# Performance work log

Hardware: AMD Instinct MI355X
Metric: run time of the kernel (lower is better)

## Reference

```python
import jax, jax.numpy as jnp
import numpy as np


def euler_xyz_to_matrix(angles):
    # pytorch3d euler_angles_to_matrix(angles, 'XYZ') = R_X(a0) @ R_Y(a1) @ R_Z(a2)
    ax, ay, az = angles[..., 0], angles[..., 1], angles[..., 2]
    cx, sx = jnp.cos(ax), jnp.sin(ax)
    cy, sy = jnp.cos(ay), jnp.sin(ay)
    cz, sz = jnp.cos(az), jnp.sin(az)
    one = jnp.ones_like(ax)
    zero = jnp.zeros_like(ax)
    Rx = jnp.stack([one, zero, zero, zero, cx, -sx, zero, sx, cx], axis=-1).reshape(*ax.shape, 3, 3)
    Ry = jnp.stack([cy, zero, sy, zero, one, zero, -sy, zero, cy], axis=-1).reshape(*ax.shape, 3, 3)
    Rz = jnp.stack([cz, -sz, zero, sz, cz, zero, zero, zero, one], axis=-1).reshape(*ax.shape, 3, 3)
    return Rx @ Ry @ Rz


def chamfer_bidir(x, y):
    # x, y: [R, I, N, 3]. Squared-distance chamfer, mean point reduction, per (R,I) batch.
    x2 = jnp.sum(x * x, axis=-1)  # [R,I,N]
    y2 = jnp.sum(y * y, axis=-1)  # [R,I,N]
    # d2[r,i,n,m] = |x_n - y_m|^2
    d2 = x2[..., :, None] + y2[..., None, :] - 2.0 * jnp.einsum('rind,rimd->rinm', x, y)
    cham_x = jnp.mean(jnp.min(d2, axis=-1), axis=-1)  # x -> nearest y
    cham_y = jnp.mean(jnp.min(d2, axis=-2), axis=-1)  # y -> nearest x
    return cham_x + cham_y  # [R, I]


def setup_inputs() -> dict:
    key = jax.random.key(0)
    k1, k2, k3, k4 = jax.random.split(key, 4)
    R, I, N = 4, 16, 2048
    source_points = jax.random.normal(k1, (R, I, N, 3), dtype=jnp.float32)
    target_points = jax.random.normal(k2, (I, N, 3), dtype=jnp.float32)
    rotation = 0.1 * jax.random.normal(k3, (R, I, 3), dtype=jnp.float32)
    translation = 0.1 * jax.random.normal(k4, (R, I, 3), dtype=jnp.float32)
    scale = jnp.ones((R, I), dtype=jnp.float32)
    return {
        'source_points': source_points,
        'target_points': target_points,
        'rotation': rotation,
        'translation': translation,
        'scale': scale,
    }


def reference(source_points, target_points, rotation, translation, scale):
    R, I, N, _ = source_points.shape
    rot = euler_xyz_to_matrix(rotation)  # [R,I,3,3]
    # Transform per original: 4x4 matrix with rows [:3,:] scaled by `scale`,
    # so p' = scale * (rot @ p + translation).
    transformed = scale[..., None, None] * (
        jnp.einsum('rind,rikd->rink', source_points, rot) + translation[..., None, :]
    )  # [R,I,N,3]
    # target_points [I,N,3] broadcast to [R,I,N,3] (original repeats along R)
    target = jnp.broadcast_to(target_points[None], transformed.shape)
    # original calls chamfer_distance(target, transformed): x=target, y=transformed
    return chamfer_bidir(target, transformed)  # [R, I]
```

## Files before the change

kernel.cpp:

```cpp
#include <hip/hip_runtime.h>
#include <math.h>

#define RDIM 4
#define IDIM 16
#define NPAIR 64
#define NPTS 2048
#define THREADS 256
#define ROWSB 256
#define RBLK (NPTS / ROWSB)
#define T16 (NPTS / 16)
#define PSPLIT 4
#define ONEBF 0x3F80u

typedef __attribute__((ext_vector_type(8))) short bf16x8;
typedef __attribute__((ext_vector_type(4))) float f32x4;

__device__ __forceinline__ float min3f(float a, float b, float c) {
    return fminf(a, fminf(b, c));
}

__device__ __forceinline__ unsigned int f2bf(float f) {
    union { float f; unsigned int u; } v; v.f = f;
    return (v.u + 0x7FFFu + ((v.u >> 16) & 1u)) >> 16;
}
__device__ __forceinline__ float bf2f(unsigned int h) {
    union { unsigned int u; float f; } v; v.u = h << 16; return v.f;
}

__device__ __forceinline__ void make_rot(const float* __restrict__ rotv, int pair,
                                         float& r00, float& r01, float& r02,
                                         float& r10, float& r11, float& r12,
                                         float& r20, float& r21, float& r22) {
    const float ax = rotv[pair * 3 + 0];
    const float ay = rotv[pair * 3 + 1];
    const float az = rotv[pair * 3 + 2];
    float sx, cx, sy, cy, sz, cz;
    sincosf(ax, &sx, &cx);
    sincosf(ay, &sy, &cy);
    sincosf(az, &sz, &cz);
    r00 = cy * cz;                r01 = -cy * sz;               r02 = sy;
    r10 = cx * sz + sx * sy * cz; r11 = cx * cz - sx * sy * sz; r12 = -sx * cy;
    r20 = sx * sz - cx * sy * cz; r21 = sx * cz + cx * sy * sz; r22 = cx * cy;
}

__device__ __forceinline__ uint4 brec(float v0, float v1, float v2) {
    const float b0 = -2.0f * v0, b1 = -2.0f * v1, b2 = -2.0f * v2;
    const unsigned int h0 = f2bf(b0), h1 = f2bf(b1), h2 = f2bf(b2);
    const unsigned int l0 = f2bf(b0 - bf2f(h0));
    const unsigned int l1 = f2bf(b1 - bf2f(h1));
    const unsigned int l2 = f2bf(b2 - bf2f(h2));
    const float n2 = v0 * v0 + v1 * v1 + v2 * v2;
    const unsigned int nh = f2bf(n2), nl = f2bf(n2 - bf2f(nh));
    return make_uint4(h0 | (h1 << 16), h2 | (l0 << 16), l1 | (l2 << 16), nh | (nl << 16));
}
__device__ __forceinline__ void arec(float q0, float q1, float q2, uint4& a0, uint4& a1) {
    const unsigned int h0 = f2bf(q0), h1 = f2bf(q1), h2 = f2bf(q2);
    const unsigned int l0 = f2bf(q0 - bf2f(h0));
    const unsigned int l1 = f2bf(q1 - bf2f(h1));
    const unsigned int l2 = f2bf(q2 - bf2f(h2));
    a0 = make_uint4(h0 | (h1 << 16), h2 | (l0 << 16), l1 | (l2 << 16), ONEBF);
    a1 = make_uint4(l0 | (l1 << 16), l2 | (h0 << 16), h1 | (h2 << 16), ONEBF << 16);
}

__global__ __launch_bounds__(THREADS)
void prep(const float* __restrict__ src, const float* __restrict__ tgt,
          const float* __restrict__ rotv, const float* __restrict__ trav,
          const float* __restrict__ scal,
          uint4* __restrict__ Yb, uint4* __restrict__ Ya,
          uint4* __restrict__ Xb, uint4* __restrict__ Xa)
{
    const int b   = blockIdx.x;
    const int seg = blockIdx.y;
    const int tid = threadIdx.x;
    const int m0  = seg * (NPTS / PSPLIT);
    if (b < NPAIR) {
        const int pair = b;
        float r00, r01, r02, r10, r11, r12, r20, r21, r22;
        make_rot(rotv, pair, r00, r01, r02, r10, r11, r12, r20, r21, r22);
        const float t0 = trav[pair * 3 + 0];
        const float t1 = trav[pair * 3 + 1];
        const float t2 = trav[pair * 3 + 2];
        const float s  = scal[pair];
        const float* __restrict__ srcp = src + (size_t)pair * NPTS * 3;
#pragma unroll
        for (int u = 0; u < NPTS / THREADS / PSPLIT; ++u) {
            const int m = m0 + u * THREADS + tid;
            const float p0 = srcp[m * 3 + 0];
            const float p1 = srcp[m * 3 + 1];
            const float p2 = srcp[m * 3 + 2];
            const float y0 = s * fmaf(r00, p0, fmaf(r01, p1, fmaf(r02, p2, t0)));
            const float y1 = s * fmaf(r10, p0, fmaf(r11, p1, fmaf(r12, p2, t1)));
            const float y2 = s * fmaf(r20, p0, fmaf(r21, p1, fmaf(r22, p2, t2)));
            Yb[(size_t)pair * NPTS + m] = brec(y0, y1, y2);
            uint4 a0, a1;
            arec(y0, y1, y2, a0, a1);
            Ya[((size_t)pair * NPTS + m) * 2 + 0] = a0;
            Ya[((size_t)pair * NPTS + m) * 2 + 1] = a1;
        }
    } else {
        const int i = b - NPAIR;
        const float* __restrict__ tgtp = tgt + (size_t)i * NPTS * 3;
#pragma unroll
        for (int u = 0; u < NPTS / THREADS / PSPLIT; ++u) {
            const int m = m0 + u * THREADS + tid;
            const float x0 = tgtp[m * 3 + 0];
            const float x1 = tgtp[m * 3 + 1];
            const float x2 = tgtp[m * 3 + 2];
            Xb[(size_t)i * NPTS + m] = brec(x0, x1, x2);
            uint4 a0, a1;
            arec(x0, x1, x2, a0, a1);
            Xa[((size_t)i * NPTS + m) * 2 + 0] = a0;
            Xa[((size_t)i * NPTS + m) * 2 + 1] = a1;
        }
    }
}

__global__ __launch_bounds__(THREADS, 4)
void chamfer_main(const uint4* __restrict__ Yb, const uint4* __restrict__ Ya,
                  const uint4* __restrict__ Xb, const uint4* __restrict__ Xa,
                  float* __restrict__ out, const float czero)
{
    __shared__ alignas(16) unsigned char smem[32768];
    __shared__ float rowmin[ROWSB];
    __shared__ float wsum[4];
    unsigned short* sB = (unsigned short*)smem;

    const int pair  = blockIdx.x;
    const int rb    = blockIdx.y;
    const int passB = blockIdx.z;
    const int i     = pair & (IDIM - 1);
    const int tid   = threadIdx.x;
    const int lane  = tid & 63;
    const int w     = tid >> 6;
    const int c15   = lane & 15;
    const int hi    = lane >> 4;

    const uint4* __restrict__ gB = (passB == 0) ? (Yb + (size_t)pair * NPTS)
                                                : (Xb + (size_t)i * NPTS);
    const uint4* __restrict__ gA = (passB == 0)
        ? (Xa + ((size_t)i * NPTS + rb * ROWSB) * 2)
        : (Ya + ((size_t)pair * NPTS + rb * ROWSB) * 2);
    const char* gAb = (const char*)gA;

#pragma unroll
    for (int j = 0; j < 8; ++j)
        ((uint4*)sB)[j * THREADS + tid] = gB[j * THREADS + tid];

    const bf16x8 zero8 = {0, 0, 0, 0, 0, 0, 0, 0};
    bf16x8 af[4];
#pragma unroll
    for (int rt = 0; rt < 4; ++rt) {
        const int row = w * 64 + rt * 16 + c15;
        af[rt] = (hi < 2) ? *(const bf16x8*)(gAb + row * 32 + hi * 16) : zero8;
    }

    f32x4 zero4;
    zero4[0] = czero; zero4[1] = czero; zero4[2] = czero; zero4[3] = czero;

    float mn[4][4];
#pragma unroll
    for (int rt = 0; rt < 4; ++rt)
#pragma unroll
        for (int j = 0; j < 4; ++j) mn[rt][j] = 3.4e38f;

    __syncthreads();

#pragma unroll 2
    for (int t = 0; t < T16; t += 2) {
        const bf16x8 bf0 = *(const bf16x8*)&sB[((t + 0) * 16 + c15) * 8];
        const bf16x8 bf1 = *(const bf16x8*)&sB[((t + 1) * 16 + c15) * 8];
#pragma unroll
        for (int rt = 0; rt < 4; ++rt) {
            const f32x4 d0 = __builtin_amdgcn_mfma_f32_16x16x32_bf16(af[rt], bf0, zero4, 0, 0, 0);
            const f32x4 d1 = __builtin_amdgcn_mfma_f32_16x16x32_bf16(af[rt], bf1, zero4, 0, 0, 0);
#pragma unroll
            for (int j = 0; j < 4; ++j)
                mn[rt][j] = min3f(mn[rt][j], d0[j], d1[j]);
        }
    }

#pragma unroll
    for (int rt = 0; rt < 4; ++rt)
#pragma unroll
        for (int j = 0; j < 4; ++j) {
            float v = mn[rt][j];
            v = fminf(v, __shfl_xor(v, 1, 64));
            v = fminf(v, __shfl_xor(v, 2, 64));
            v = fminf(v, __shfl_xor(v, 4, 64));
            v = fminf(v, __shfl_xor(v, 8, 64));
            mn[rt][j] = v;
        }

    if (c15 == 0) {
#pragma unroll
        for (int rt = 0; rt < 4; ++rt) {
            f32x4 v4;
            v4[0] = mn[rt][0]; v4[1] = mn[rt][1];
            v4[2] = mn[rt][2]; v4[3] = mn[rt][3];
            *(f32x4*)&rowmin[w * 64 + rt * 16 + hi * 4] = v4;
        }
    }
    __syncthreads();

    const float m = rowmin[tid];
    const unsigned short* ar = (const unsigned short*)(gAb + tid * 32);
    const float q0 = bf2f(ar[0]) + bf2f(ar[3]);
    const float q1 = bf2f(ar[1]) + bf2f(ar[4]);
    const float q2 = bf2f(ar[2]) + bf2f(ar[5]);
    float v = m + q0 * q0 + q1 * q1 + q2 * q2;

#pragma unroll
    for (int off = 32; off > 0; off >>= 1)
        v += __shfl_down(v, off, 64);
    if (lane == 0) wsum[w] = v;
    __syncthreads();
    if (tid == 0) {
        const float tot = wsum[0] + wsum[1] + wsum[2] + wsum[3];
        atomicAdd(&out[pair], tot * (1.0f / NPTS));
    }
}

extern "C" void kernel_launch(void* const* d_in, const int* in_sizes, int n_in,
                              void* d_out, int out_size, void* d_ws, size_t ws_size,
                              hipStream_t stream) {
    const float* src  = (const float*)d_in[0];
    const float* tgt  = (const float*)d_in[1];
    const float* rotv = (const float*)d_in[2];
    const float* trav = (const float*)d_in[3];
    const float* scal = (const float*)d_in[4];
    float* out = (float*)d_out;

    char* ws = (char*)d_ws;
    uint4* Yb = (uint4*)ws;
    uint4* Ya = (uint4*)(ws + (size_t)NPAIR * NPTS * 16);
    uint4* Xb = (uint4*)(ws + (size_t)NPAIR * NPTS * 48);
    uint4* Xa = (uint4*)(ws + (size_t)NPAIR * NPTS * 48 + (size_t)IDIM * NPTS * 16);

    hipMemsetAsync(out, 0, NPAIR * sizeof(float), stream);

    dim3 pgrid(NPAIR + IDIM, PSPLIT);
    prep<<<pgrid, THREADS, 0, stream>>>(src, tgt, rotv, trav, scal, Yb, Ya, Xb, Xa);

    dim3 grid(NPAIR, RBLK, 2);
    chamfer_main<<<grid, THREADS, 0, stream>>>(Yb, Ya, Xb, Xa, out, 0.0f);
}
```

Baseline: 105.5 us.

## Switch chamfer MFMA to 32x32x16 tiles with software-pipelined min reduction

Result: faster. 85.79 us (median of 2 runs) (-18.7%).

```diff
diff --git a/kernel.cpp b/kernel.cpp
--- a/kernel.cpp
+++ b/kernel.cpp
@@ -8,11 +8,12 @@
 #define THREADS 256
 #define ROWSB 256
 #define RBLK (NPTS / ROWSB)
-#define T16 (NPTS / 16)
+#define TILES (NPTS / 32)
 #define PSPLIT 4
 #define ONEBF 0x3F80u
 
 typedef __attribute__((ext_vector_type(8))) short bf16x8;
+typedef __attribute__((ext_vector_type(16))) float f32x16;
 typedef __attribute__((ext_vector_type(4))) float f32x4;
 
 __device__ __forceinline__ float min3f(float a, float b, float c) {
@@ -67,11 +68,13 @@
           const float* __restrict__ rotv, const float* __restrict__ trav,
           const float* __restrict__ scal,
           uint4* __restrict__ Yb, uint4* __restrict__ Ya,
-          uint4* __restrict__ Xb, uint4* __restrict__ Xa)
+          uint4* __restrict__ Xb, uint4* __restrict__ Xa,
+          float* __restrict__ out)
 {
     const int b   = blockIdx.x;
     const int seg = blockIdx.y;
     const int tid = threadIdx.x;
+    if (b == 0 && seg == 0 && tid < NPAIR) out[tid] = 0.0f;
     const int m0  = seg * (NPTS / PSPLIT);
     if (b < NPAIR) {
         const int pair = b;
@@ -115,7 +118,7 @@
     }
 }
 
-__global__ __launch_bounds__(THREADS, 4)
+__global__ __launch_bounds__(THREADS, 3)
 void chamfer_main(const uint4* __restrict__ Yb, const uint4* __restrict__ Ya,
                   const uint4* __restrict__ Xb, const uint4* __restrict__ Xa,
                   float* __restrict__ out, const float czero)
@@ -132,8 +135,8 @@
     const int tid   = threadIdx.x;
     const int lane  = tid & 63;
     const int w     = tid >> 6;
-    const int c15   = lane & 15;
-    const int hi    = lane >> 4;
+    const int c31   = lane & 31;
+    const int h     = lane >> 5;
 
     const uint4* __restrict__ gB = (passB == 0) ? (Yb + (size_t)pair * NPTS)
                                                 : (Xb + (size_t)i * NPTS);
@@ -146,58 +149,73 @@
     for (int j = 0; j < 8; ++j)
         ((uint4*)sB)[j * THREADS + tid] = gB[j * THREADS + tid];
 
-    const bf16x8 zero8 = {0, 0, 0, 0, 0, 0, 0, 0};
-    bf16x8 af[4];
-#pragma unroll
-    for (int rt = 0; rt < 4; ++rt) {
-        const int row = w * 64 + rt * 16 + c15;
-        af[rt] = (hi < 2) ? *(const bf16x8*)(gAb + row * 32 + hi * 16) : zero8;
-    }
-
-    f32x4 zero4;
-    zero4[0] = czero; zero4[1] = czero; zero4[2] = czero; zero4[3] = czero;
-
-    float mn[4][4];
-#pragma unroll
-    for (int rt = 0; rt < 4; ++rt)
-#pragma unroll
-        for (int j = 0; j < 4; ++j) mn[rt][j] = 3.4e38f;
+    const bf16x8 af0 = *(const bf16x8*)(gAb + (w * 64 + c31) * 32 + h * 16);
+    const bf16x8 af1 = *(const bf16x8*)(gAb + (w * 64 + 32 + c31) * 32 + h * 16);
+
+    f32x16 czv;
+#pragma unroll
+    for (int j = 0; j < 16; ++j) czv[j] = czero;
+
+    float mn0[16], mn1[16];
+#pragma unroll
+    for (int j = 0; j < 16; ++j) { mn0[j] = 3.4e38f; mn1[j] = 3.4e38f; }
 
     __syncthreads();
 
-#pragma unroll 2
-    for (int t = 0; t < T16; t += 2) {
-        const bf16x8 bf0 = *(const bf16x8*)&sB[((t + 0) * 16 + c15) * 8];
-        const bf16x8 bf1 = *(const bf16x8*)&sB[((t + 1) * 16 + c15) * 8];
-#pragma unroll
-        for (int rt = 0; rt < 4; ++rt) {
-            const f32x4 d0 = __builtin_amdgcn_mfma_f32_16x16x32_bf16(af[rt], bf0, zero4, 0, 0, 0);
-            const f32x4 d1 = __builtin_amdgcn_mfma_f32_16x16x32_bf16(af[rt], bf1, zero4, 0, 0, 0);
-#pragma unroll
-            for (int j = 0; j < 4; ++j)
-                mn[rt][j] = min3f(mn[rt][j], d0[j], d1[j]);
-        }
-    }
-
-#pragma unroll
-    for (int rt = 0; rt < 4; ++rt)
-#pragma unroll
-        for (int j = 0; j < 4; ++j) {
-            float v = mn[rt][j];
-            v = fminf(v, __shfl_xor(v, 1, 64));
-            v = fminf(v, __shfl_xor(v, 2, 64));
-            v = fminf(v, __shfl_xor(v, 4, 64));
-            v = fminf(v, __shfl_xor(v, 8, 64));
-            mn[rt][j] = v;
-        }
-
-    if (c15 == 0) {
-#pragma unroll
-        for (int rt = 0; rt < 4; ++rt) {
-            f32x4 v4;
-            v4[0] = mn[rt][0]; v4[1] = mn[rt][1];
-            v4[2] = mn[rt][2]; v4[3] = mn[rt][3];
-            *(f32x4*)&rowmin[w * 64 + rt * 16 + hi * 4] = v4;
+    bf16x8 bfA = *(const bf16x8*)&sB[(0 * 32 + c31) * 8];
+    bf16x8 bfB = *(const bf16x8*)&sB[(1 * 32 + c31) * 8];
+    f32x16 a0  = __builtin_amdgcn_mfma_f32_32x32x16_bf16(af0, bfA, czv, 0, 0, 0);
+    f32x16 b0  = __builtin_amdgcn_mfma_f32_32x32x16_bf16(af0, bfB, czv, 0, 0, 0);
+    f32x16 pa1 = __builtin_amdgcn_mfma_f32_32x32x16_bf16(af1, bfA, czv, 0, 0, 0);
+    f32x16 pb1 = __builtin_amdgcn_mfma_f32_32x32x16_bf16(af1, bfB, czv, 0, 0, 0);
+#pragma unroll
+    for (int j = 0; j < 16; ++j)
+        mn0[j] = min3f(mn0[j], a0[j], b0[j]);
+
+    for (int t = 2; t < TILES; t += 2) {
+        bfA = *(const bf16x8*)&sB[((t + 0) * 32 + c31) * 8];
+        bfB = *(const bf16x8*)&sB[((t + 1) * 32 + c31) * 8];
+        a0 = __builtin_amdgcn_mfma_f32_32x32x16_bf16(af0, bfA, czv, 0, 0, 0);
+        b0 = __builtin_amdgcn_mfma_f32_32x32x16_bf16(af0, bfB, czv, 0, 0, 0);
+#pragma unroll
+        for (int j = 0; j < 16; ++j)
+            mn1[j] = min3f(mn1[j], pa1[j], pb1[j]);
+        pa1 = __builtin_amdgcn_mfma_f32_32x32x16_bf16(af1, bfA, czv, 0, 0, 0);
+        pb1 = __builtin_amdgcn_mfma_f32_32x32x16_bf16(af1, bfB, czv, 0, 0, 0);
+#pragma unroll
+        for (int j = 0; j < 16; ++j)
+            mn0[j] = min3f(mn0[j], a0[j], b0[j]);
+    }
+#pragma unroll
+    for (int j = 0; j < 16; ++j)
+        mn1[j] = min3f(mn1[j], pa1[j], pb1[j]);
+
+#pragma unroll
+    for (int j = 0; j < 16; ++j) {
+        float v0 = mn0[j], v1 = mn1[j];
+        v0 = fminf(v0, __shfl_xor(v0, 1, 64));
+        v1 = fminf(v1, __shfl_xor(v1, 1, 64));
+        v0 = fminf(v0, __shfl_xor(v0, 2, 64));
+        v1 = fminf(v1, __shfl_xor(v1, 2, 64));
+        v0 = fminf(v0, __shfl_xor(v0, 4, 64));
+        v1 = fminf(v1, __shfl_xor(v1, 4, 64));
+        v0 = fminf(v0, __shfl_xor(v0, 8, 64));
+        v1 = fminf(v1, __shfl_xor(v1, 8, 64));
+        v0 = fminf(v0, __shfl_xor(v0, 16, 64));
+        v1 = fminf(v1, __shfl_xor(v1, 16, 64));
+        mn0[j] = v0; mn1[j] = v1;
+    }
+
+    if (c31 == 0) {
+#pragma unroll
+        for (int g = 0; g < 4; ++g) {
+            f32x4 v4, u4;
+            v4[0] = mn0[g * 4 + 0]; v4[1] = mn0[g * 4 + 1];
+            v4[2] = mn0[g * 4 + 2]; v4[3] = mn0[g * 4 + 3];
+            u4[0] = mn1[g * 4 + 0]; u4[1] = mn1[g * 4 + 1];
+            u4[2] = mn1[g * 4 + 2]; u4[3] = mn1[g * 4 + 3];
+            *(f32x4*)&rowmin[w * 64 + 8 * g + 4 * h] = v4;
+            *(f32x4*)&rowmin[w * 64 + 32 + 8 * g + 4 * h] = u4;
         }
     }
     __syncthreads();
@@ -236,10 +254,8 @@
     uint4* Xb = (uint4*)(ws + (size_t)NPAIR * NPTS * 48);
     uint4* Xa = (uint4*)(ws + (size_t)NPAIR * NPTS * 48 + (size_t)IDIM * NPTS * 16);
 
-    hipMemsetAsync(out, 0, NPAIR * sizeof(float), stream);
-
     dim3 pgrid(NPAIR + IDIM, PSPLIT);
-    prep<<<pgrid, THREADS, 0, stream>>>(src, tgt, rotv, trav, scal, Yb, Ya, Xb, Xa);
+    prep<<<pgrid, THREADS, 0, stream>>>(src, tgt, rotv, trav, scal, Yb, Ya, Xb, Xa, out);
 
     dim3 grid(NPAIR, RBLK, 2);
     chamfer_main<<<grid, THREADS, 0, stream>>>(Yb, Ya, Xb, Xa, out, 0.0f);
```
